# Performance work log

Hardware: AMD Instinct MI355X
Metric: run time of the kernel (lower is better)

Reference implementation:

```python
import jax, jax.numpy as jnp
import numpy as np

NUM_CLUSTERS = 256


def setup_inputs() -> dict:
    key = jax.random.key(0)
    k1, k2, k3 = jax.random.split(key, 3)
    a, b, k = 8192, 8192, NUM_CLUSTERS
    w_mat = jax.random.uniform(k1, (a, b), dtype=jnp.float32)
    # softmax-like assignment probabilities over clusters
    p_l = jax.nn.softmax(jax.random.normal(k2, (a, k), dtype=jnp.float32), axis=-1)
    p_r = jax.nn.softmax(jax.random.normal(k3, (b, k), dtype=jnp.float32), axis=-1)
    clusters_p = jnp.ones((k,), dtype=jnp.float32) / k  # uniform init as in module
    return {"w_mat": w_mat, "p_l": p_l, "p_r": p_r, "clusters_p": clusters_p}


def reference(w_mat, p_l, p_r, clusters_p):
    # Algebraically equivalent to:
    #   ((w[:,:,None] * (p_l[:,None,:] + p_r[None,:,:] - 2*p_l[:,None,:]*p_r[None,:,:]))
    #      .sum((0,1)) / clusters_p).sum()
    # without materializing the (a,b,k) tensor.
    row_w = jnp.sum(w_mat, axis=1)            # (a,)  sum_b w[a,b]
    col_w = jnp.sum(w_mat, axis=0)            # (b,)  sum_a w[a,b]
    rs = row_w @ p_l                           # (k,)  sum_{a,b} w * p_l
    cs = col_w @ p_r                           # (k,)  sum_{a,b} w * p_r
    # cross[k] = sum_{a,b} p_l[a,k] * w[a,b] * p_r[b,k]
    cross = jnp.einsum("ka,ak->k", p_l.T @ w_mat, p_r)  # (k,)
    return jnp.sum((rs + cs - 2.0 * cross) / clusters_p)
```

## Files before the change

### kernel.cpp

```cpp
#include <hip/hip_runtime.h>
#include <stdint.h>

#define A_DIM 8192
#define B_DIM 8192
#define K_CL  256
#define BM    64
#define BK    64
#define NSLAB 4
#define SLABW (B_DIM / NSLAB)
#define NKS   (SLABW / BK)

typedef short bf16x8 __attribute__((ext_vector_type(8)));
typedef float f32x4  __attribute__((ext_vector_type(4)));
typedef float f32x16 __attribute__((ext_vector_type(16)));
typedef unsigned short u16;

__device__ __forceinline__ u16 f2bf(float f) {
    unsigned int u = __float_as_uint(f);
    u += 0x7fffu + ((u >> 16) & 1u);
    return (u16)(u >> 16);
}

__global__ __launch_bounds__(256) void k_prep(const float* __restrict__ pr,
                                              u16* __restrict__ Bpack,
                                              float* __restrict__ out) {
    const int kb2 = blockIdx.x;
    const int t = threadIdx.x;
    if (kb2 == 0 && t == 0) out[0] = 0.0f;
    const int lane = t & 63, wv = t >> 6;
    const int l31 = lane & 31, half = lane >> 5;
#pragma unroll
    for (int ci = 0; ci < 2; ci++) {
        const int c2 = wv * 2 + ci;
        float v[8];
#pragma unroll
        for (int j = 0; j < 8; j++)
            v[j] = pr[(size_t)(kb2 * 16 + half * 8 + j) * K_CL + c2 * 32 + l31];
        union { bf16x8 b; unsigned int u[4]; } o;
#pragma unroll
        for (int j = 0; j < 4; j++)
            o.u[j] = (unsigned int)f2bf(v[2 * j]) | ((unsigned int)f2bf(v[2 * j + 1]) << 16);
        *(bf16x8*)(Bpack + ((size_t)(kb2 * 8 + c2) * 64 + lane) * 8) = o.b;
    }
}

__global__ __launch_bounds__(256, 2) void k_main(const float* __restrict__ w,
                                                 const float* __restrict__ pl,
                                                 const u16* __restrict__ Bpack,
                                                 const float* __restrict__ cp,
                                                 float* __restrict__ out) {
    __shared__ float Abuf[4][BM * BK];
    __shared__ float rowsum[BM];
    __shared__ float red[4];

    const int bid = blockIdx.x;
    const int slab = bid & 3;
    const int m0 = (bid >> 2) * BM;
    const int tid = threadIdx.x;
    const int lane = tid & 63, wv = tid >> 6;
    const int l31 = lane & 31, half = lane >> 5;
    const int kb2base = slab * 128;

    if (tid < BM) rowsum[tid] = 0.0f;

    float rcp_cp[2];
#pragma unroll
    for (int n2 = 0; n2 < 2; n2++)
        rcp_cp[n2] = 1.0f / cp[wv * 64 + n2 * 32 + l31];

    __syncthreads();

    const char* wbase = (const char*)(w + (size_t)m0 * B_DIM + (size_t)slab * SLABW);

    auto stage = [&](int buf, int ks) {
#pragma unroll
        for (int i = 0; i < 4; i++) {
            const int r4 = tid >> 4;
            const int sw = r4 << 4;
            const char* src = wbase + (size_t)(i * 16 + r4) * (B_DIM * 4) + ks * 256 + (((tid & 15) * 16) ^ sw);
            void* dst = (void*)&Abuf[buf][i * 1024 + (tid >> 4) * 64 + (tid & 15) * 4];
            __builtin_amdgcn_global_load_lds(
                (const __attribute__((address_space(1))) void*)src,
                (__attribute__((address_space(3))) void*)dst, 16, 0, 0);
        }
    };

#define LOADB(arr, ks) do {                                                              \
        _Pragma("unroll")                                                                \
        for (int kf_ = 0; kf_ < 4; kf_++)                                                \
            _Pragma("unroll")                                                            \
            for (int n2_ = 0; n2_ < 2; n2_++)                                            \
                (arr)[kf_ * 2 + n2_] = *(const bf16x8*)(Bpack +                          \
                    (((size_t)(kb2base + (ks) * 4 + kf_) * 8 + wv * 2 + n2_) * 64 + lane) * 8); \
    } while (0)

#define COMPUTE(cur, arr) do {                                                           \
        const char* abase_ = (const char*)&Abuf[(cur)][0];                               \
        const int sw_ = (l31 & 15) << 4;                                                 \
        _Pragma("unroll")                                                                \
        for (int kf_ = 0; kf_ < 4; kf_++) {                                              \
            bf16x8 a_[2];                                                                \
            f32x4 f0_[2], f1_[2];                                                        \
            _Pragma("unroll")                                                            \
            for (int mf_ = 0; mf_ < 2; mf_++) {                                          \
                const char* rp_ = abase_ + (mf_ * 32 + l31) * 256;                       \
                f0_[mf_] = *(const f32x4*)(rp_ + ((kf_ * 64 + half * 32) ^ sw_));        \
                f1_[mf_] = *(const f32x4*)(rp_ + ((kf_ * 64 + half * 32 + 16) ^ sw_));   \
                union { bf16x8 v; unsigned int u[4]; } pa_;                              \
                pa_.u[0] = __builtin_amdgcn_perm(__float_as_uint(f0_[mf_][1]), __float_as_uint(f0_[mf_][0]), 0x07060302u); \
                pa_.u[1] = __builtin_amdgcn_perm(__float_as_uint(f0_[mf_][3]), __float_as_uint(f0_[mf_][2]), 0x07060302u); \
                pa_.u[2] = __builtin_amdgcn_perm(__float_as_uint(f1_[mf_][1]), __float_as_uint(f1_[mf_][0]), 0x07060302u); \
                pa_.u[3] = __builtin_amdgcn_perm(__float_as_uint(f1_[mf_][3]), __float_as_uint(f1_[mf_][2]), 0x07060302u); \
                a_[mf_] = pa_.v;                                                         \
            }                                                                            \
            if (kf_ == wv) {                \
                sums0 += f0_[0][0]+f0_[0][1]+f0_[0][2]+f0_[0][3]+f1_[0][0]+f1_[0][1]+f1_[0][2]+f1_[0][3]; \
                sums1 += f0_[1][0]+f0_[1][1]+f0_[1][2]+f0_[1][3]+f1_[1][0]+f1_[1][1]+f1_[1][2]+f1_[1][3]; \
            }                                                                            \
            _Pragma("unroll")                                                            \
            for (int mf_ = 0; mf_ < 2; mf_++)                                            \
                _Pragma("unroll")                                                        \
                for (int n2_ = 0; n2_ < 2; n2_++)                                        \
                    acc[mf_ * 2 + n2_] = __builtin_amdgcn_mfma_f32_32x32x16_bf16(        \
                        a_[mf_], (arr)[kf_ * 2 + n2_], acc[mf_ * 2 + n2_], 0, 0, 0);     \
        }                                                                                \
    } while (0)

#define BODY(ks, WAITN, BCUR, BNXT, DOSTAGE, DOLOADB) do {                               \
        asm volatile("s_waitcnt vmcnt(" #WAITN ")" ::: "memory");                        \
        __builtin_amdgcn_s_barrier();                                                    \
        __builtin_amdgcn_sched_barrier(0);                                               \
        if (DOLOADB) LOADB(BNXT, (ks) + 1);                                              \
        if (DOSTAGE) stage(((ks) + 3) & 3, (ks) + 3);                                    \
        COMPUTE((ks) & 3, BCUR);                                                         \
    } while (0)

    f32x16 acc[4];
#pragma unroll
    for (int i = 0; i < 4; i++)
#pragma unroll
        for (int r = 0; r < 16; r++) acc[i][r] = 0.f;
    float sums0 = 0.f, sums1 = 0.f;

    bf16x8 bA[8], bB[8];
    stage(0, 0); stage(1, 1); stage(2, 2);
    LOADB(bA, 0);

    for (int ks = 0; ks < NKS - 4; ks += 2) {
        BODY(ks,     16, bA, bB, 1, 1);
        BODY(ks + 1, 16, bB, bA, 1, 1);
    }
    BODY(28, 16, bA, bB, 1, 1);
    BODY(29, 16, bB, bA, 0, 1);
    BODY(30, 12, bA, bB, 0, 1);
    BODY(31,  8, bB, bA, 0, 0);

#undef BODY
#undef COMPUTE
#undef LOADB

    {
        float v0 = sums0 + __shfl_xor(sums0, 32, 64);
        float v1 = sums1 + __shfl_xor(sums1, 32, 64);
        if (lane < 32) {
            atomicAdd(&rowsum[l31], v0);
            atomicAdd(&rowsum[32 + l31], v1);
        }
    }
    __syncthreads();

    float tot = 0.f;
#pragma unroll
    for (int mf = 0; mf < 2; mf++) {
#pragma unroll
        for (int reg = 0; reg < 16; reg++) {
            const int lrow = mf * 32 + (reg & 3) + 8 * (reg >> 2) + 4 * half;
            const float rs = rowsum[lrow];
            const float* plrow = pl + (size_t)(m0 + lrow) * K_CL + wv * 64 + l31;
#pragma unroll
            for (int n2 = 0; n2 < 2; n2++) {
                const float q = acc[mf * 2 + n2][reg];
                const float p = plrow[n2 * 32];
                tot += (q + p * (rs - 2.0f * q)) * rcp_cp[n2];
            }
        }
    }
    for (int o = 32; o; o >>= 1) tot += __shfl_down(tot, o, 64);
    if (lane == 0) red[wv] = tot;
    __syncthreads();
    if (tid == 0) atomicAdd(out, red[0] + red[1] + red[2] + red[3]);
}

extern "C" void kernel_launch(void* const* d_in, const int* in_sizes, int n_in,
                              void* d_out, int out_size, void* d_ws, size_t ws_size,
                              hipStream_t stream) {
    const float* w  = (const float*)d_in[0];
    const float* pl = (const float*)d_in[1];
    const float* pr = (const float*)d_in[2];
    const float* cp = (const float*)d_in[3];
    float* out = (float*)d_out;

    u16* Bpack = (u16*)d_ws;

    k_prep<<<dim3(512), dim3(256), 0, stream>>>(pr, Bpack, out);
    k_main<<<dim3(128 * NSLAB), dim3(256), 0, stream>>>(w, pl, Bpack, cp, out);
}
```

Baseline: 74.83 us.

## Convert W tile to bf16 once via registers before staging in LDS

Replaces the direct global-to-LDS fp32 staging with a register path. Each thread loads its fp32 W chunk, computes the row-sum contribution, converts the chunk to bf16 once and writes it to a double-buffered, XOR-swizzled bf16 LDS tile. The MFMA loop then reads bf16 fragments directly, so the repeated per-wave fp32 LDS reads and conversions disappear, and the LDS footprint drops to a quarter. The cost is more VGPRs for in-flight loads, an extra barrier per step, and a shallower prefetch depth.

```diff
diff --git a/kernel.cpp b/kernel.cpp
--- a/kernel.cpp
+++ b/kernel.cpp
@@ -13,6 +13,7 @@
 typedef short bf16x8 __attribute__((ext_vector_type(8)));
 typedef float f32x4  __attribute__((ext_vector_type(4)));
 typedef float f32x16 __attribute__((ext_vector_type(16)));
+typedef unsigned int uint4v __attribute__((ext_vector_type(4)));
 typedef unsigned short u16;
 
 __device__ __forceinline__ u16 f2bf(float f) {
@@ -49,7 +50,7 @@
                                                  const u16* __restrict__ Bpack,
                                                  const float* __restrict__ cp,
                                                  float* __restrict__ out) {
-    __shared__ float Abuf[4][BM * BK];
+    __shared__ u16 Abf[2][BM * BK];
     __shared__ float rowsum[BM];
     __shared__ float red[4];
 
@@ -61,29 +62,32 @@
     const int l31 = lane & 31, half = lane >> 5;
     const int kb2base = slab * 128;
 
-    if (tid < BM) rowsum[tid] = 0.0f;
+    const int srow = wv * 16 + (lane >> 2);
+    const int scg  = lane & 3;
+    const float* wthr = w + (size_t)(m0 + srow) * B_DIM + (size_t)slab * SLABW + scg * 16;
+
+    const int wb0 = srow * 128 + ((scg * 32)      ^ ((srow & 7) << 4));
+    const int wb1 = srow * 128 + ((scg * 32 + 16) ^ ((srow & 7) << 4));
 
     float rcp_cp[2];
 #pragma unroll
     for (int n2 = 0; n2 < 2; n2++)
         rcp_cp[n2] = 1.0f / cp[wv * 64 + n2 * 32 + l31];
 
-    __syncthreads();
-
-    const char* wbase = (const char*)(w + (size_t)m0 * B_DIM + (size_t)slab * SLABW);
-
-    auto stage = [&](int buf, int ks) {
-#pragma unroll
-        for (int i = 0; i < 4; i++) {
-            const int r4 = tid >> 4;
-            const int sw = r4 << 4;
-            const char* src = wbase + (size_t)(i * 16 + r4) * (B_DIM * 4) + ks * 256 + (((tid & 15) * 16) ^ sw);
-            void* dst = (void*)&Abuf[buf][i * 1024 + (tid >> 4) * 64 + (tid & 15) * 4];
-            __builtin_amdgcn_global_load_lds(
-                (const __attribute__((address_space(1))) void*)src,
-                (__attribute__((address_space(3))) void*)dst, 16, 0, 0);
-        }
-    };
+    f32x16 acc[4];
+#pragma unroll
+    for (int i = 0; i < 4; i++)
+#pragma unroll
+        for (int r = 0; r < 16; r++) acc[i][r] = 0.f;
+    float sums = 0.f;
+
+#define GLOAD(R, ks) do {                                                                \
+        const float* gp_ = wthr + (size_t)(ks) * BK;                                     \
+        R##0 = *(const f32x4*)(gp_);                                                     \
+        R##1 = *(const f32x4*)(gp_ + 4);                                                 \
+        R##2 = *(const f32x4*)(gp_ + 8);                                                 \
+        R##3 = *(const f32x4*)(gp_ + 12);                                                \
+    } while (0)
 
 #define LOADB(arr, ks) do {                                                              \
         _Pragma("unroll")                                                                \
@@ -94,78 +98,80 @@
                     (((size_t)(kb2base + (ks) * 4 + kf_) * 8 + wv * 2 + n2_) * 64 + lane) * 8); \
     } while (0)
 
+#define PERM2(hi, lo) __builtin_amdgcn_perm(__float_as_uint(hi), __float_as_uint(lo), 0x07060302u)
+
+#define CONVERT(R, buf) do {                                                             \
+        sums += R##0[0]+R##0[1]+R##0[2]+R##0[3] + R##1[0]+R##1[1]+R##1[2]+R##1[3]        \
+              + R##2[0]+R##2[1]+R##2[2]+R##2[3] + R##3[0]+R##3[1]+R##3[2]+R##3[3];       \
+        uint4v w0_, w1_;                                                                 \
+        w0_[0] = PERM2(R##0[1], R##0[0]); w0_[1] = PERM2(R##0[3], R##0[2]);              \
+        w0_[2] = PERM2(R##1[1], R##1[0]); w0_[3] = PERM2(R##1[3], R##1[2]);              \
+        w1_[0] = PERM2(R##2[1], R##2[0]); w1_[1] = PERM2(R##2[3], R##2[2]);              \
+        w1_[2] = PERM2(R##3[1], R##3[0]); w1_[3] = PERM2(R##3[3], R##3[2]);              \
+        *(uint4v*)((char*)&Abf[(buf)][0] + wb0) = w0_;                                   \
+        *(uint4v*)((char*)&Abf[(buf)][0] + wb1) = w1_;                                   \
+    } while (0)
+
 #define COMPUTE(cur, arr) do {                                                           \
-        const char* abase_ = (const char*)&Abuf[(cur)][0];                               \
-        const int sw_ = (l31 & 15) << 4;                                                 \
+        const char* ab_ = (const char*)&Abf[(cur)][0];                                   \
+        const int sx_ = (l31 & 7) << 4;                                                  \
         _Pragma("unroll")                                                                \
         for (int kf_ = 0; kf_ < 4; kf_++) {                                              \
-            bf16x8 a_[2];                                                                \
-            f32x4 f0_[2], f1_[2];                                                        \
-            _Pragma("unroll")                                                            \
-            for (int mf_ = 0; mf_ < 2; mf_++) {                                          \
-                const char* rp_ = abase_ + (mf_ * 32 + l31) * 256;                       \
-                f0_[mf_] = *(const f32x4*)(rp_ + ((kf_ * 64 + half * 32) ^ sw_));        \
-                f1_[mf_] = *(const f32x4*)(rp_ + ((kf_ * 64 + half * 32 + 16) ^ sw_));   \
-                union { bf16x8 v; unsigned int u[4]; } pa_;                              \
-                pa_.u[0] = __builtin_amdgcn_perm(__float_as_uint(f0_[mf_][1]), __float_as_uint(f0_[mf_][0]), 0x07060302u); \
-                pa_.u[1] = __builtin_amdgcn_perm(__float_as_uint(f0_[mf_][3]), __float_as_uint(f0_[mf_][2]), 0x07060302u); \
-                pa_.u[2] = __builtin_amdgcn_perm(__float_as_uint(f1_[mf_][1]), __float_as_uint(f1_[mf_][0]), 0x07060302u); \
-                pa_.u[3] = __builtin_amdgcn_perm(__float_as_uint(f1_[mf_][3]), __float_as_uint(f1_[mf_][2]), 0x07060302u); \
-                a_[mf_] = pa_.v;                                                         \
-            }                                                                            \
-            if (kf_ == wv) {                \
-                sums0 += f0_[0][0]+f0_[0][1]+f0_[0][2]+f0_[0][3]+f1_[0][0]+f1_[0][1]+f1_[0][2]+f1_[0][3]; \
-                sums1 += f0_[1][0]+f0_[1][1]+f0_[1][2]+f0_[1][3]+f1_[1][0]+f1_[1][1]+f1_[1][2]+f1_[1][3]; \
-            }                                                                            \
-            _Pragma("unroll")                                                            \
-            for (int mf_ = 0; mf_ < 2; mf_++)                                            \
-                _Pragma("unroll")                                                        \
-                for (int n2_ = 0; n2_ < 2; n2_++)                                        \
-                    acc[mf_ * 2 + n2_] = __builtin_amdgcn_mfma_f32_32x32x16_bf16(        \
-                        a_[mf_], (arr)[kf_ * 2 + n2_], acc[mf_ * 2 + n2_], 0, 0, 0);     \
+            bf16x8 a0_ = *(const bf16x8*)(ab_ + (l31 * 128        + ((kf_ * 32 + half * 16) ^ sx_))); \
+            bf16x8 a1_ = *(const bf16x8*)(ab_ + ((32 + l31) * 128 + ((kf_ * 32 + half * 16) ^ sx_))); \
+            acc[0] = __builtin_amdgcn_mfma_f32_32x32x16_bf16(a0_, (arr)[kf_ * 2 + 0], acc[0], 0, 0, 0); \
+            acc[1] = __builtin_amdgcn_mfma_f32_32x32x16_bf16(a0_, (arr)[kf_ * 2 + 1], acc[1], 0, 0, 0); \
+            acc[2] = __builtin_amdgcn_mfma_f32_32x32x16_bf16(a1_, (arr)[kf_ * 2 + 0], acc[2], 0, 0, 0); \
+            acc[3] = __builtin_amdgcn_mfma_f32_32x32x16_bf16(a1_, (arr)[kf_ * 2 + 1], acc[3], 0, 0, 0); \
         }                                                                                \
     } while (0)
 
-#define BODY(ks, WAITN, BCUR, BNXT, DOSTAGE, DOLOADB) do {                               \
+#define BODYX(ks, WAITN, BC, BN, RC, RN, DOB, DOG, DOCONV, DOBAR) do {                   \
+        if (DOB) LOADB(BN, (ks) + 1);                                                    \
+        if (DOG) GLOAD(RN, (ks) + 2);                                                    \
         asm volatile("s_waitcnt vmcnt(" #WAITN ")" ::: "memory");                        \
-        __builtin_amdgcn_s_barrier();                                                    \
         __builtin_amdgcn_sched_barrier(0);                                               \
-        if (DOLOADB) LOADB(BNXT, (ks) + 1);                                              \
-        if (DOSTAGE) stage(((ks) + 3) & 3, (ks) + 3);                                    \
-        COMPUTE((ks) & 3, BCUR);                                                         \
-    } while (0)
-
-    f32x16 acc[4];
-#pragma unroll
-    for (int i = 0; i < 4; i++)
-#pragma unroll
-        for (int r = 0; r < 16; r++) acc[i][r] = 0.f;
-    float sums0 = 0.f, sums1 = 0.f;
-
+        if (DOCONV) CONVERT(RC, ((ks) + 1) & 1);                                         \
+        COMPUTE((ks) & 1, BC);                                                           \
+        if (DOBAR) {                                                                     \
+            asm volatile("s_waitcnt lgkmcnt(0)" ::: "memory");                           \
+            __builtin_amdgcn_s_barrier();                                                \
+            __builtin_amdgcn_sched_barrier(0);                                           \
+        }                                                                                \
+    } while (0)
+
+    f32x4 rA0, rA1, rA2, rA3, rB0, rB1, rB2, rB3;
     bf16x8 bA[8], bB[8];
-    stage(0, 0); stage(1, 1); stage(2, 2);
+
+    GLOAD(rA, 0);
     LOADB(bA, 0);
-
-    for (int ks = 0; ks < NKS - 4; ks += 2) {
-        BODY(ks,     16, bA, bB, 1, 1);
-        BODY(ks + 1, 16, bB, bA, 1, 1);
-    }
-    BODY(28, 16, bA, bB, 1, 1);
-    BODY(29, 16, bB, bA, 0, 1);
-    BODY(30, 12, bA, bB, 0, 1);
-    BODY(31,  8, bB, bA, 0, 0);
-
-#undef BODY
+    GLOAD(rB, 1);
+    asm volatile("s_waitcnt vmcnt(12)" ::: "memory");
+    __builtin_amdgcn_sched_barrier(0);
+    CONVERT(rA, 0);
+    asm volatile("s_waitcnt lgkmcnt(0)" ::: "memory");
+    __builtin_amdgcn_s_barrier();
+    __builtin_amdgcn_sched_barrier(0);
+
+    for (int ks = 0; ks < NKS - 2; ks += 2) {
+        BODYX(ks,     12, bA, bB, rB, rA, 1, 1, 1, 1);
+        BODYX(ks + 1, 12, bB, bA, rA, rB, 1, 1, 1, 1);
+    }
+    BODYX(30, 8, bA, bB, rB, rA, 1, 0, 1, 1);
+    BODYX(31, 0, bB, bA, rA, rB, 0, 0, 0, 0);
+
+#undef BODYX
 #undef COMPUTE
+#undef CONVERT
+#undef PERM2
 #undef LOADB
+#undef GLOAD
 
     {
-        float v0 = sums0 + __shfl_xor(sums0, 32, 64);
-        float v1 = sums1 + __shfl_xor(sums1, 32, 64);
-        if (lane < 32) {
-            atomicAdd(&rowsum[l31], v0);
-            atomicAdd(&rowsum[32 + l31], v1);
-        }
+        float v = sums;
+        v += __shfl_xor(v, 1, 64);
+        v += __shfl_xor(v, 2, 64);
+        if ((lane & 3) == 0) rowsum[srow] = v;
     }
     __syncthreads();
 
```

Result: faster. 72.28 us (-3.4%).
